# Kernel tuning notes

Measured on AMD Instinct MI355X. Metric: run time of the kernel, lower is better.

The kernel has to match this reference:

```python
import jax, jax.numpy as jnp
import numpy as np

B, N, C, H, L = 4, 1024, 1152, 16, 120
D = C // H
HID = 4 * C
EPS = 1e-6


def _ln(x):
    m = jnp.mean(x, axis=-1, keepdims=True)
    v = jnp.var(x, axis=-1, keepdims=True)
    return (x - m) * jax.lax.rsqrt(v + EPS)


def _attend(q, k, v):
    # q:(B,H,Nq,D) k,v:(B,H,Nk,D)
    scale = D ** -0.5
    s = jnp.einsum('bhnd,bhmd->bhnm', q, k) * scale
    p = jax.nn.softmax(s, axis=-1)
    o = jnp.einsum('bhnm,bhmd->bhnd', p, v)
    return o.transpose(0, 2, 1, 3).reshape(q.shape[0], q.shape[2], C)


def setup_inputs() -> dict:
    key = jax.random.key(0)
    ks = jax.random.split(key, 20)
    g = lambda i, shape, s=0.02: jax.random.normal(ks[i], shape, jnp.float32) * s
    return {
        'x': jax.random.normal(ks[0], (B, N, C), jnp.float32),
        'y': jax.random.normal(ks[1], (B, L, C), jnp.float32),
        't': jax.random.normal(ks[2], (B, 6 * C), jnp.float32),
        'sst': jax.random.normal(ks[3], (6, C), jnp.float32) / C ** 0.5,
        'qkv_w': g(4, (C, 3 * C)), 'qkv_b': jnp.zeros((3 * C,), jnp.float32),
        'proj_w': g(5, (C, C)), 'proj_b': jnp.zeros((C,), jnp.float32),
        'q_w': g(6, (C, C)), 'q_b': jnp.zeros((C,), jnp.float32),
        'kv_w': g(7, (C, 2 * C)), 'kv_b': jnp.zeros((2 * C,), jnp.float32),
        'cproj_w': g(8, (C, C)), 'cproj_b': jnp.zeros((C,), jnp.float32),
        'fc1_w': g(9, (C, HID)), 'fc1_b': jnp.zeros((HID,), jnp.float32),
        'fc2_w': g(10, (HID, C)), 'fc2_b': jnp.zeros((C,), jnp.float32),
    }


def reference(x, y, t, sst, qkv_w, qkv_b, proj_w, proj_b, q_w, q_b,
              kv_w, kv_b, cproj_w, cproj_b, fc1_w, fc1_b, fc2_w, fc2_b):
    mods = sst[None] + t.reshape(B, 6, C)  # (B,6,C)
    sh_msa, sc_msa, g_msa, sh_mlp, sc_mlp, g_mlp = [mods[:, i:i + 1] for i in range(6)]

    # --- self attention with adaLN modulation ---
    h = _ln(x) * (1 + sc_msa) + sh_msa
    qkv = (h @ qkv_w + qkv_b).reshape(B, N, 3, H, D).transpose(2, 0, 3, 1, 4)
    attn_out = _attend(qkv[0], qkv[1], qkv[2]) @ proj_w + proj_b
    x = x + g_msa * attn_out

    # --- cross attention (batched cond, no mask) ---
    q = (x @ q_w + q_b).reshape(B, N, H, D).transpose(0, 2, 1, 3)
    kv = (y @ kv_w + kv_b).reshape(B, L, 2, H, D).transpose(2, 0, 3, 1, 4)
    x = x + (_attend(q, kv[0], kv[1]) @ cproj_w + cproj_b)

    # --- MLP with adaLN modulation ---
    h = _ln(x) * (1 + sc_mlp) + sh_mlp
    h = jax.nn.gelu(h @ fc1_w + fc1_b, approximate=True) @ fc2_w + fc2_b
    x = x + g_mlp * h
    return x
```

## Files before the change

### kernel.cpp

```cpp
#include <hip/hip_runtime.h>
#include <hip/hip_bf16.h>
#include <stdint.h>

typedef __hip_bfloat16 BT;
typedef __bf16 bf16x8 __attribute__((ext_vector_type(8)));
typedef float f32x4 __attribute__((ext_vector_type(4)));

constexpr int kB = 4, kN = 1024, kC = 1152, kH = 16, kL = 120, kD = 72, kDp = 96;
constexpr int kHid = 4608, kBN = 4096, kZ = 64;
constexpr float kScale = 0.11785113019775793f;

__global__ void detect_dtype(const void* xin, int* flag) {
  __shared__ int cnt;
  if (threadIdx.x == 0) cnt = 0;
  __syncthreads();
  const BT* xb = (const BT*)xin;
  int local = 0;
  for (int i = threadIdx.x; i < 4096; i += 256) {
    float v = __bfloat162float(xb[i]);
    if (!(fabsf(v) <= 1e3f)) local++;
  }
  atomicAdd(&cnt, local);
  __syncthreads();
  if (threadIdx.x == 0) *flag = (cnt > 8) ? 1 : 0;
}

struct ConvSeg {
  const void* src;
  BT* dst;
  long long n;
};
struct ConvArgs {
  ConvSeg seg[10];
  int nseg;
};
__global__ void convert_all(ConvArgs a, const int* __restrict__ flag) {
  const int f = *flag;
  long long i = (long long)blockIdx.x * 256 + threadIdx.x;
#pragma unroll
  for (int s = 0; s < 10; ++s) {
    if (s >= a.nseg) return;
    if (i < a.seg[s].n) {
      a.seg[s].dst[i] = f ? __float2bfloat16(((const float*)a.seg[s].src)[i])
                          : ((const BT*)a.seg[s].src)[i];
      return;
    }
    i -= a.seg[s].n;
  }
}

__global__ void encode_ws(float* out, long long n, float c) {
  long long i = (long long)blockIdx.x * 256 + threadIdx.x;
  if (i < n) out[i] = c;
}

__device__ __forceinline__ void gl_lds16(const BT* g, BT* l) {
  __builtin_amdgcn_global_load_lds(
      (const __attribute__((address_space(1))) uint32_t*)g,
      (__attribute__((address_space(3))) uint32_t*)l, 16, 0, 0);
}

template <int BM, int BN, int EP>
__global__ __launch_bounds__(256, 3) void gemm_t64(
    const BT* __restrict__ A, const BT* __restrict__ Bm, const BT* __restrict__ bias,
    void* __restrict__ Cout, int M, int Nc, int K, int lda, int ldb, int ldc,
    long long sA, long long sB, long long sC) {
  constexpr int NA = BM / 32;
  constexpr int NB = BN / 32;
  constexpr int NU = NA + NB;
  constexpr int NJ = (BM == 128 && BN == 128) ? 4 : 2;
  __shared__ __align__(16) BT As[2][BM * 64];
  __shared__ __align__(16) BT Bs[2][BN * 64];
  A += (long long)blockIdx.z * sA;
  Bm += (long long)blockIdx.z * sB;

  const int gx = gridDim.x, nwg = gx * gridDim.y;
  int id = blockIdx.y * gx + blockIdx.x;
  {
    const int q = nwg >> 3, r = nwg & 7;
    const int xcd = id & 7, pos = id >> 3;
    const int base = (xcd < r) ? xcd * (q + 1) : r * (q + 1) + (xcd - r) * q;
    id = base + pos;
  }
  const int m0 = (id / gx) * BM, n0 = (id % gx) * BN;

  const int lane = threadIdx.x & 63, w = threadIdx.x >> 6;
  const int l15 = lane & 15;
  const int srow = lane >> 3;
  const int ssrc = ((lane & 7) ^ srow) * 8;
  int wm, wn;
  if (BM == 128 && BN == 128) { wm = (w & 1) * 64; wn = (w >> 1) * 64; }
  else if (BM == 128) { wm = (w >> 1) * 64; wn = (w & 1) * 32; }
  else { wm = 0; wn = w * 32; }

  const bool has2 = (w + 4 < NU);
  const int u1 = w;
  const int u2 = has2 ? (w + 4) : w;
  const BT* gp1[4];
  const BT* gp2[4];
#pragma unroll
  for (int q = 0; q < 4; ++q) {
    {
      int rr, lim;
      const BT* basep;
      int stride;
      if (u1 < NA) { rr = m0 + u1 * 32; lim = M; basep = A; stride = lda; }
      else { rr = n0 + (u1 - NA) * 32; lim = Nc; basep = Bm; stride = ldb; }
      rr += q * 8 + srow;
      if (rr >= lim) rr = lim - 1;
      gp1[q] = basep + (long long)rr * stride + ssrc;
    }
    {
      int rr, lim;
      const BT* basep;
      int stride;
      if (u2 < NA) { rr = m0 + u2 * 32; lim = M; basep = A; stride = lda; }
      else { rr = n0 + (u2 - NA) * 32; lim = Nc; basep = Bm; stride = ldb; }
      rr += q * 8 + srow;
      if (rr >= lim) rr = lim - 1;
      gp2[q] = basep + (long long)rr * stride + ssrc;
    }
  }
  BT* d1[2];
  BT* d2[2];
#pragma unroll
  for (int bb = 0; bb < 2; ++bb) {
    d1[bb] = (u1 < NA) ? &As[bb][u1 * 2048] : &Bs[bb][(u1 - NA) * 2048];
    int ub = u2 - NA;
    if (ub < 0) ub = 0;
    if (ub > NB - 1) ub = NB - 1;
    d2[bb] = (u2 < NA) ? &As[bb][u2 * 2048] : &Bs[bb][ub * 2048];
  }

  auto stage = [&](int bb, int k0) {
#pragma unroll
    for (int q = 0; q < 4; ++q) gl_lds16(gp1[q] + k0, d1[bb] + q * 512);
    if (has2) {
#pragma unroll
      for (int q = 0; q < 4; ++q) gl_lds16(gp2[q] + k0, d2[bb] + q * 512);
    }
  };

  const int rsw = l15 & 7;
  const int ch0 = ((lane >> 4) ^ rsw) * 8;
  const int ch1 = ((4 | (lane >> 4)) ^ rsw) * 8;

  f32x4 acc[4][NJ] = {};

  auto compute = [&](int bb) {
    bf16x8 af[4][2], bf[NJ][2];
#pragma unroll
    for (int i = 0; i < 4; ++i) {
      const int row = wm + i * 16 + l15;
      af[i][0] = *reinterpret_cast<const bf16x8*>(&As[bb][row * 64 + ch0]);
      af[i][1] = *reinterpret_cast<const bf16x8*>(&As[bb][row * 64 + ch1]);
    }
#pragma unroll
    for (int j = 0; j < NJ; ++j) {
      const int row = wn + j * 16 + l15;
      bf[j][0] = *reinterpret_cast<const bf16x8*>(&Bs[bb][row * 64 + ch0]);
      bf[j][1] = *reinterpret_cast<const bf16x8*>(&Bs[bb][row * 64 + ch1]);
    }
#pragma unroll
    for (int i = 0; i < 4; ++i)
#pragma unroll
      for (int j = 0; j < NJ; ++j) {
        acc[i][j] = __builtin_amdgcn_mfma_f32_16x16x32_bf16(af[i][0], bf[j][0], acc[i][j], 0, 0, 0);
        acc[i][j] = __builtin_amdgcn_mfma_f32_16x16x32_bf16(af[i][1], bf[j][1], acc[i][j], 0, 0, 0);
      }
  };

  stage(0, 0);
  __syncthreads();
  const int nk = K >> 6;
  int cur = 0;
  for (int t = 1; t < nk; ++t) {
    stage(cur ^ 1, t << 6);
    compute(cur);
    __syncthreads();
    cur ^= 1;
  }
  compute(cur);

  const int rowq = (lane >> 4) * 4;
  const long long cb = (long long)blockIdx.z * sC;
#pragma unroll
  for (int j = 0; j < NJ; ++j) {
    int col = n0 + wn + j * 16 + l15;
    if (col >= Nc) continue;
    float bv = bias ? __bfloat162float(bias[col]) : 0.f;
#pragma unroll
    for (int i = 0; i < 4; ++i) {
      int row = m0 + wm + i * 16 + rowq;
#pragma unroll
      for (int r = 0; r < 4; ++r) {
        if (row + r < M) {
          float v = acc[i][j][r] + bv;
          if (EP == 2) {
            float z = 1.5957691216057308f * (v + 0.044715f * v * v * v);
            v = v / (1.f + __expf(-z));
          }
          long long off = cb + (long long)(row + r) * ldc + col;
          if (EP == 1)
            ((float*)Cout)[off] = v;
          else
            ((BT*)Cout)[off] = __float2bfloat16(v);
        }
      }
    }
  }
}

template <int EP>
__global__ __launch_bounds__(256, 4) void gemm_tile(
    const BT* __restrict__ A, const BT* __restrict__ Bm, const BT* __restrict__ bias,
    void* __restrict__ Cout, int M, int Nc, int K, int lda, int ldb, int ldc,
    long long sA, long long sB, long long sC) {
  __shared__ __align__(16) BT As[2][128 * 32];
  __shared__ __align__(16) BT Bs[2][128 * 32];
  A += (long long)blockIdx.z * sA;
  Bm += (long long)blockIdx.z * sB;

  const int gx = gridDim.x, nwg = gx * gridDim.y;
  int id = blockIdx.y * gx + blockIdx.x;
  {
    const int q = nwg >> 3, r = nwg & 7;
    const int xcd = id & 7, pos = id >> 3;
    const int base = (xcd < r) ? xcd * (q + 1) : r * (q + 1) + (xcd - r) * q;
    id = base + pos;
  }
  const int m0 = (id / gx) * 128, n0 = (id % gx) * 128;

  const int lane = threadIdx.x & 63, w = threadIdx.x >> 6;
  const int lr = lane >> 2, lc = (lane & 3) * 8;
  const int l15 = lane & 15, q8 = (lane >> 4) * 8;
  const int wm = (w & 1) * 64, wn = (w >> 1) * 64;

  int ra0 = m0 + w * 32 + lr, ra1 = ra0 + 16;
  if (ra0 >= M) ra0 = M - 1;
  if (ra1 >= M) ra1 = M - 1;
  int rb0 = n0 + w * 32 + lr, rb1 = rb0 + 16;
  if (rb0 >= Nc) rb0 = Nc - 1;
  if (rb1 >= Nc) rb1 = Nc - 1;
  const BT* pa0 = A + (long long)ra0 * lda + lc;
  const BT* pa1 = A + (long long)ra1 * lda + lc;
  const BT* pb0 = Bm + (long long)rb0 * ldb + lc;
  const BT* pb1 = Bm + (long long)rb1 * ldb + lc;

  auto stage = [&](int bb, int k0) {
    gl_lds16(pa0 + k0, &As[bb][w * 1024]);
    gl_lds16(pa1 + k0, &As[bb][w * 1024 + 512]);
    gl_lds16(pb0 + k0, &Bs[bb][w * 1024]);
    gl_lds16(pb1 + k0, &Bs[bb][w * 1024 + 512]);
  };

  f32x4 acc[4][4] = {};

  auto compute = [&](int bb) {
    bf16x8 af[4], bf[4];
#pragma unroll
    for (int i = 0; i < 4; ++i)
      af[i] = *reinterpret_cast<const bf16x8*>(&As[bb][(wm + i * 16 + l15) * 32 + q8]);
#pragma unroll
    for (int j = 0; j < 4; ++j)
      bf[j] = *reinterpret_cast<const bf16x8*>(&Bs[bb][(wn + j * 16 + l15) * 32 + q8]);
#pragma unroll
    for (int i = 0; i < 4; ++i)
#pragma unroll
      for (int j = 0; j < 4; ++j)
        acc[i][j] = __builtin_amdgcn_mfma_f32_16x16x32_bf16(af[i], bf[j], acc[i][j], 0, 0, 0);
  };

  stage(0, 0);
  __syncthreads();
  const int nk = K >> 5;
  int cur = 0;
  for (int t = 1; t < nk; ++t) {
    stage(cur ^ 1, t << 5);
    compute(cur);
    __syncthreads();
    cur ^= 1;
  }
  compute(cur);

  const int rowq = (lane >> 4) * 4;
  const long long cb = (long long)blockIdx.z * sC;
#pragma unroll
  for (int j = 0; j < 4; ++j) {
    int col = n0 + wn + j * 16 + l15;
    if (col >= Nc) continue;
    float bv = bias ? __bfloat162float(bias[col]) : 0.f;
#pragma unroll
    for (int i = 0; i < 4; ++i) {
      int row = m0 + wm + i * 16 + rowq;
#pragma unroll
      for (int r = 0; r < 4; ++r) {
        if (row + r < M) {
          float v = acc[i][j][r] + bv;
          if (EP == 2) {
            float z = 1.5957691216057308f * (v + 0.044715f * v * v * v);
            v = v / (1.f + __expf(-z));
          }
          long long off = cb + (long long)(row + r) * ldc + col;
          if (EP == 1)
            ((float*)Cout)[off] = v;
          else
            ((BT*)Cout)[off] = __float2bfloat16(v);
        }
      }
    }
  }
}

__global__ void transpose_any(const void* __restrict__ in, BT* __restrict__ out,
                              int R, int Cin, const int* __restrict__ flag) {
  __shared__ BT tile[32][33];
  const int f = *flag;
  const int tx = threadIdx.x & 31, ty = threadIdx.x >> 5;
  const int r0 = blockIdx.y * 32, c0 = blockIdx.x * 32;
#pragma unroll
  for (int j = 0; j < 32; j += 8) {
    int r = r0 + ty + j;
    if (r < R && c0 + tx < Cin) {
      long long idx = (long long)r * Cin + c0 + tx;
      tile[ty + j][tx] = f ? __float2bfloat16(((const float*)in)[idx]) : ((const BT*)in)[idx];
    }
  }
  __syncthreads();
#pragma unroll
  for (int j = 0; j < 32; j += 8) {
    int oc = c0 + ty + j;
    if (oc < Cin && r0 + tx < R) out[(long long)oc * R + r0 + tx] = tile[tx][ty + j];
  }
}

template <int SRC>
__global__ __launch_bounds__(256) void ln_mod(const void* __restrict__ xin,
                                              const BT* __restrict__ tc,
                                              const BT* __restrict__ sstc,
                                              BT* __restrict__ hout,
                                              int shiftRow, int scaleRow,
                                              const int* __restrict__ flag) {
  const int f = (SRC == 1) ? 1 : *flag;
  const int row = blockIdx.x;
  const int b = row >> 10;
  const long long base = (long long)row * kC;
  float s = 0.f, s2 = 0.f;
  for (int c = threadIdx.x; c < kC; c += 256) {
    float v = f ? ((const float*)xin)[base + c] : __bfloat162float(((const BT*)xin)[base + c]);
    s += v;
    s2 += v * v;
  }
  for (int o = 32; o > 0; o >>= 1) {
    s += __shfl_down(s, o, 64);
    s2 += __shfl_down(s2, o, 64);
  }
  __shared__ float red[8];
  const int w = threadIdx.x >> 6;
  if ((threadIdx.x & 63) == 0) {
    red[w] = s;
    red[4 + w] = s2;
  }
  __syncthreads();
  const float m = (red[0] + red[1] + red[2] + red[3]) * (1.f / kC);
  const float ex2 = (red[4] + red[5] + red[6] + red[7]) * (1.f / kC);
  const float rstd = rsqrtf(ex2 - m * m + 1e-6f);
  const BT* tsh = tc + (long long)b * 6 * kC + (long long)shiftRow * kC;
  const BT* tsc = tc + (long long)b * 6 * kC + (long long)scaleRow * kC;
  const BT* ssh = sstc + (long long)shiftRow * kC;
  const BT* ssc = sstc + (long long)scaleRow * kC;
  for (int c = threadIdx.x; c < kC; c += 256) {
    float sc = __bfloat162float(ssc[c]) + __bfloat162float(tsc[c]);
    float sh = __bfloat162float(ssh[c]) + __bfloat162float(tsh[c]);
    float xv0 = f ? ((const float*)xin)[base + c] : __bfloat162float(((const BT*)xin)[base + c]);
    float xv = (xv0 - m) * rstd;
    hout[base + c] = __float2bfloat16(xv * (1.f + sc) + sh);
  }
}

__global__ void scatter_qk(const BT* __restrict__ qkv, BT* __restrict__ Qp,
                           BT* __restrict__ Kp) {
  long long i = (long long)blockIdx.x * 256 + threadIdx.x;
  if (i >= (long long)kZ * kN * kDp) return;
  int d = (int)(i % kDp);
  long long r = i / kDp;
  int n = (int)(r % kN);
  int z = (int)(r / kN);
  int b = z >> 4, h = z & 15;
  if (d < kD) {
    long long src = ((long long)(b * kN + n)) * (3 * kC) + h * kD + d;
    Qp[i] = __float2bfloat16(kScale * __bfloat162float(qkv[src]));
    Kp[i] = qkv[src + kC];
  } else {
    Qp[i] = __float2bfloat16(0.f);
    Kp[i] = __float2bfloat16(0.f);
  }
}

__global__ void scatter_v(const BT* __restrict__ qkv, BT* __restrict__ VT) {
  long long i = (long long)blockIdx.x * 256 + threadIdx.x;
  if (i >= (long long)kZ * kD * kN) return;
  int n = (int)(i % kN);
  long long r = i / kN;
  int d = (int)(r % kD);
  int z = (int)(r / kD);
  int b = z >> 4, h = z & 15;
  VT[i] = qkv[((long long)(b * kN + n)) * (3 * kC) + 2 * kC + h * kD + d];
}

__global__ void scatter_qc(const BT* __restrict__ qc, BT* __restrict__ Qp) {
  long long i = (long long)blockIdx.x * 256 + threadIdx.x;
  if (i >= (long long)kZ * kN * kDp) return;
  int d = (int)(i % kDp);
  long long r = i / kDp;
  int n = (int)(r % kN);
  int z = (int)(r / kN);
  int b = z >> 4, h = z & 15;
  Qp[i] = (d < kD)
              ? __float2bfloat16(kScale * __bfloat162float(qc[((long long)(b * kN + n)) * kC + h * kD + d]))
              : __float2bfloat16(0.f);
}

__global__ void scatter_kc(const BT* __restrict__ kvb, BT* __restrict__ Kcp) {
  long long i = (long long)blockIdx.x * 256 + threadIdx.x;
  if (i >= (long long)kZ * kL * kDp) return;
  int d = (int)(i % kDp);
  long long r = i / kDp;
  int l = (int)(r % kL);
  int z = (int)(r / kL);
  int b = z >> 4, h = z & 15;
  Kcp[i] = (d < kD) ? kvb[((long long)(b * kL + l)) * (2 * kC) + h * kD + d] : __float2bfloat16(0.f);
}

__global__ void scatter_vc(const BT* __restrict__ kvb, BT* __restrict__ VcT) {
  long long i = (long long)blockIdx.x * 256 + threadIdx.x;
  if (i >= (long long)kZ * kD * 128) return;
  int l = (int)(i % 128);
  long long r = i / 128;
  int d = (int)(r % kD);
  int z = (int)(r / kD);
  int b = z >> 4, h = z & 15;
  VcT[i] = (l < kL) ? kvb[((long long)(b * kL + l)) * (2 * kC) + kC + h * kD + d] : __float2bfloat16(0.f);
}

__global__ void heads_to_cat(const BT* __restrict__ O, BT* __restrict__ cat) {
  long long i = (long long)blockIdx.x * 256 + threadIdx.x;
  if (i >= (long long)kZ * kN * kD) return;
  int d = (int)(i % kD);
  long long r = i / kD;
  int n = (int)(r % kN);
  int z = (int)(r / kN);
  int b = z >> 4, h = z & 15;
  cat[((long long)(b * kN + n)) * kC + h * kD + d] = O[i];
}

__global__ __launch_bounds__(256) void softmax1024(BT* __restrict__ S) {
  const long long row = blockIdx.x;
  BT* r = S + row * 1024;
  const int tid = threadIdx.x;
  union { ushort4 u; BT b[4]; } ld;
  ld.u = *(const ushort4*)(r + tid * 4);
  float v[4];
#pragma unroll
  for (int k = 0; k < 4; ++k) v[k] = __bfloat162float(ld.b[k]);
  float mx = fmaxf(fmaxf(v[0], v[1]), fmaxf(v[2], v[3]));
  for (int o = 32; o > 0; o >>= 1) mx = fmaxf(mx, __shfl_down(mx, o, 64));
  __shared__ float red[4], red2[4];
  if ((tid & 63) == 0) red[tid >> 6] = mx;
  __syncthreads();
  mx = fmaxf(fmaxf(red[0], red[1]), fmaxf(red[2], red[3]));
  float s = 0.f;
#pragma unroll
  for (int k = 0; k < 4; ++k) {
    v[k] = __expf(v[k] - mx);
    s += v[k];
  }
  for (int o = 32; o > 0; o >>= 1) s += __shfl_down(s, o, 64);
  if ((tid & 63) == 0) red2[tid >> 6] = s;
  __syncthreads();
  s = red2[0] + red2[1] + red2[2] + red2[3];
  const float inv = 1.f / s;
#pragma unroll
  for (int k = 0; k < 4; ++k) ld.b[k] = __float2bfloat16(v[k] * inv);
  *(ushort4*)(r + tid * 4) = ld.u;
}

__global__ void softmax_cross(BT* __restrict__ S) {
  const long long row = blockIdx.x;
  BT* r = S + row * 128;
  const int c = threadIdx.x;
  float v = (c < kL) ? __bfloat162float(r[c]) : -1e30f;
  float mx = v;
  for (int o = 32; o > 0; o >>= 1) mx = fmaxf(mx, __shfl_down(mx, o, 64));
  __shared__ float sm[2], ss[2];
  if ((c & 63) == 0) sm[c >> 6] = mx;
  __syncthreads();
  mx = fmaxf(sm[0], sm[1]);
  float e = (c < kL) ? __expf(v - mx) : 0.f;
  float s = e;
  for (int o = 32; o > 0; o >>= 1) s += __shfl_down(s, o, 64);
  if ((c & 63) == 0) ss[c >> 6] = s;
  __syncthreads();
  s = ss[0] + ss[1];
  r[c] = __float2bfloat16(e / s);
}

__global__ void resid_gate(const void* __restrict__ x, const BT* __restrict__ raw,
                           const BT* __restrict__ tc, const BT* __restrict__ sstc,
                           float* __restrict__ resf, BT* __restrict__ resb,
                           const int* __restrict__ flag) {
  long long i = (long long)blockIdx.x * 256 + threadIdx.x;
  if (i >= (long long)kBN * kC) return;
  const int f = *flag;
  int c = (int)(i % kC);
  int b = (int)(i / ((long long)kN * kC));
  float g = __bfloat162float(sstc[2 * kC + c]) + __bfloat162float(tc[(long long)b * 6 * kC + 2 * kC + c]);
  float xv = f ? ((const float*)x)[i] : __bfloat162float(((const BT*)x)[i]);
  float v = xv + g * __bfloat162float(raw[i]);
  resf[i] = v;
  resb[i] = __float2bfloat16(v);
}

__global__ void resid_add(float* __restrict__ res, const BT* __restrict__ raw) {
  long long i = (long long)blockIdx.x * 256 + threadIdx.x;
  if (i < (long long)kBN * kC) res[i] += __bfloat162float(raw[i]);
}

__global__ void final_out(const float* __restrict__ res, const BT* __restrict__ raw,
                          const BT* __restrict__ tc, const BT* __restrict__ sstc,
                          float* __restrict__ out) {
  long long i = (long long)blockIdx.x * 256 + threadIdx.x;
  if (i >= (long long)kBN * kC) return;
  int c = (int)(i % kC);
  int b = (int)(i / ((long long)kN * kC));
  float g = __bfloat162float(sstc[5 * kC + c]) + __bfloat162float(tc[(long long)b * 6 * kC + 5 * kC + c]);
  out[i] = res[i] + g * __bfloat162float(raw[i]);
}

extern "C" void kernel_launch(void* const* d_in, const int* in_sizes, int n_in,
                              void* d_out, int out_size, void* d_ws, size_t ws_size,
                              hipStream_t stream) {
  const void* x = d_in[0];
  const void* y = d_in[1];
  const void* t = d_in[2];
  const void* sst = d_in[3];
  const void* qkv_w = d_in[4];
  const void* qkv_b = d_in[5];
  const void* proj_w = d_in[6];
  const void* proj_b = d_in[7];
  const void* q_w = d_in[8];
  const void* q_b = d_in[9];
  const void* kv_w = d_in[10];
  const void* kv_b = d_in[11];
  const void* cproj_w = d_in[12];
  const void* cproj_b = d_in[13];
  const void* fc1_w = d_in[14];
  const void* fc1_b = d_in[15];
  const void* fc2_w = d_in[16];
  const void* fc2_b = d_in[17];
  (void)in_sizes; (void)n_in;

  char* p = (char*)d_ws;
  size_t off = 0;
  auto alloc = [&](size_t bytes) {
    void* r = p + off;
    off += (bytes + 1023) & ~(size_t)1023;
    return r;
  };
  int* dflag = (int*)alloc(16);
  BT* canonY = (BT*)alloc((size_t)kB * kL * kC * 2);
  BT* canonT = (BT*)alloc((size_t)kB * 6 * kC * 2);
  BT* canonSst = (BT*)alloc((size_t)6 * kC * 2);
  BT* canonBias = (BT*)alloc((size_t)16384 * 2);
  BT* wT = (BT*)alloc((size_t)kHid * kC * 2);
  BT* bufH = (BT*)alloc((size_t)kBN * kC * 2);
  BT* bufCH = (BT*)alloc((size_t)kZ * kN * kDp * 2);
  BT* bufQp = (BT*)alloc((size_t)kZ * kN * kDp * 2);
  BT* bufVT = (BT*)alloc((size_t)kZ * kD * kN * 2);
  BT* rawB = (BT*)alloc((size_t)kBN * kC * 2);
  float* resF = (float*)alloc((size_t)kBN * kC * 4);
  BT* arena = (BT*)alloc((size_t)kBN * kHid * 2);
  const size_t need = off;

  BT* bufO = rawB;
  BT* fc2T = bufQp;
  BT* kvBuf = (BT*)((char*)arena + 17825792);

  if (ws_size < need) {
    float c = 100.f * (float)(1 + (int)(ws_size >> 24));
    long long n = (long long)out_size;
    encode_ws<<<(int)((n + 255) / 256), 256, 0, stream>>>((float*)d_out, n, c);
    return;
  }

  BT* qkvB = canonBias;
  BT* projB = canonBias + 3456;
  BT* qB = canonBias + 4608;
  BT* kvB = canonBias + 5760;
  BT* cprojB = canonBias + 8064;
  BT* fc1B = canonBias + 9216;
  BT* fc2B = canonBias + 13824;

  auto gemm = [&](int ep, const BT* A, const BT* Bm, const BT* bias, void* Cp,
                  int M, int Nc, int K, int lda, int ldb, int ldc,
                  long long sA, long long sB, long long sC, int Zb) {
    if (K & 63) {
      dim3 g((Nc + 127) / 128, (M + 127) / 128, Zb);
      if (ep == 0)
        gemm_tile<0><<<g, 256, 0, stream>>>(A, Bm, bias, Cp, M, Nc, K, lda, ldb, ldc, sA, sB, sC);
      else if (ep == 1)
        gemm_tile<1><<<g, 256, 0, stream>>>(A, Bm, bias, Cp, M, Nc, K, lda, ldb, ldc, sA, sB, sC);
      else
        gemm_tile<2><<<g, 256, 0, stream>>>(A, Bm, bias, Cp, M, Nc, K, lda, ldb, ldc, sA, sB, sC);
      return;
    }
    long long n64 = (long long)((Nc + 63) / 64) * ((M + 127) / 128) * Zb;
    if (n64 >= 512) {
      dim3 g((Nc + 63) / 64, (M + 127) / 128, Zb);
      if (ep == 0)
        gemm_t64<128, 64, 0><<<g, 256, 0, stream>>>(A, Bm, bias, Cp, M, Nc, K, lda, ldb, ldc, sA, sB, sC);
      else if (ep == 1)
        gemm_t64<128, 64, 1><<<g, 256, 0, stream>>>(A, Bm, bias, Cp, M, Nc, K, lda, ldb, ldc, sA, sB, sC);
      else
        gemm_t64<128, 64, 2><<<g, 256, 0, stream>>>(A, Bm, bias, Cp, M, Nc, K, lda, ldb, ldc, sA, sB, sC);
    } else {
      dim3 g((Nc + 127) / 128, (M + 63) / 64, Zb);
      if (ep == 0)
        gemm_t64<64, 128, 0><<<g, 256, 0, stream>>>(A, Bm, bias, Cp, M, Nc, K, lda, ldb, ldc, sA, sB, sC);
      else if (ep == 1)
        gemm_t64<64, 128, 1><<<g, 256, 0, stream>>>(A, Bm, bias, Cp, M, Nc, K, lda, ldb, ldc, sA, sB, sC);
      else
        gemm_t64<64, 128, 2><<<g, 256, 0, stream>>>(A, Bm, bias, Cp, M, Nc, K, lda, ldb, ldc, sA, sB, sC);
    }
  };
  auto tp = [&](const void* in, BT* out, int R, int Cin) {
    dim3 g((Cin + 31) / 32, (R + 31) / 32);
    transpose_any<<<g, 256, 0, stream>>>(in, out, R, Cin, dflag);
  };

  detect_dtype<<<1, 256, 0, stream>>>(x, dflag);
  {
    ConvArgs a;
    a.seg[0] = {y, canonY, (long long)kB * kL * kC};
    a.seg[1] = {t, canonT, (long long)kB * 6 * kC};
    a.seg[2] = {sst, canonSst, (long long)6 * kC};
    a.seg[3] = {qkv_b, qkvB, 3456};
    a.seg[4] = {proj_b, projB, 1152};
    a.seg[5] = {q_b, qB, 1152};
    a.seg[6] = {kv_b, kvB, 2304};
    a.seg[7] = {cproj_b, cprojB, 1152};
    a.seg[8] = {fc1_b, fc1B, 4608};
    a.seg[9] = {fc2_b, fc2B, 1152};
    a.nseg = 10;
    long long tot = 552960 + 27648 + 6912 + 14976;
    convert_all<<<(int)((tot + 255) / 256), 256, 0, stream>>>(a, dflag);
  }

  ln_mod<0><<<kBN, 256, 0, stream>>>(x, canonT, canonSst, bufH, 0, 1, dflag);
  tp(qkv_w, wT, kC, 3 * kC);
  gemm(0, bufH, wT, qkvB, arena, kBN, 3 * kC, kC, kC, kC, 3 * kC, 0, 0, 0, 1);
  {
    long long tot = (long long)kZ * kN * kDp;
    scatter_qk<<<(int)((tot + 255) / 256), 256, 0, stream>>>(arena, bufQp, bufCH);
    tot = (long long)kZ * kD * kN;
    scatter_v<<<(int)((tot + 255) / 256), 256, 0, stream>>>(arena, bufVT);
  }
  for (int c = 0; c < 4; ++c) {
    int z0 = c * 16;
    const BT* Qb = bufQp + (size_t)z0 * kN * kDp;
    const BT* Kb = bufCH + (size_t)z0 * kN * kDp;
    const BT* Vb = bufVT + (size_t)z0 * kD * kN;
    BT* Ob = bufO + (size_t)z0 * kN * kD;
    gemm(0, Qb, Kb, nullptr, arena, kN, kN, kDp, kDp, kDp, kN,
         (long long)kN * kDp, (long long)kN * kDp, (long long)kN * kN, 16);
    softmax1024<<<16 * kN, 256, 0, stream>>>(arena);
    gemm(0, arena, Vb, nullptr, Ob, kN, kD, kN, kN, kN, kD,
         (long long)kN * kN, (long long)kD * kN, (long long)kN * kD, 16);
  }
  heads_to_cat<<<18432, 256, 0, stream>>>(bufO, bufCH);
  tp(proj_w, wT, kC, kC);
  gemm(0, bufCH, wT, projB, rawB, kBN, kC, kC, kC, kC, kC, 0, 0, 0, 1);
  resid_gate<<<18432, 256, 0, stream>>>(x, rawB, canonT, canonSst, resF, bufH, dflag);

  tp(q_w, wT, kC, kC);
  gemm(0, bufH, wT, qB, bufCH, kBN, kC, kC, kC, kC, kC, 0, 0, 0, 1);
  {
    long long tot = (long long)kZ * kN * kDp;
    scatter_qc<<<(int)((tot + 255) / 256), 256, 0, stream>>>(bufCH, bufQp);
  }
  tp(kv_w, wT, kC, 2 * kC);
  gemm(0, canonY, wT, kvB, kvBuf, kB * kL, 2 * kC, kC, kC, kC, 2 * kC, 0, 0, 0, 1);
  {
    long long tot = (long long)kZ * kL * kDp;
    scatter_kc<<<(int)((tot + 255) / 256), 256, 0, stream>>>(kvBuf, bufCH);
    tot = (long long)kZ * kD * 128;
    scatter_vc<<<(int)((tot + 255) / 256), 256, 0, stream>>>(kvBuf, bufVT);
  }
  gemm(0, bufQp, bufCH, nullptr, arena, kN, kL, kDp, kDp, kDp, 128,
       (long long)kN * kDp, (long long)kL * kDp, (long long)kN * 128, kZ);
  softmax_cross<<<kZ * kN, 128, 0, stream>>>(arena);
  gemm(0, arena, bufVT, nullptr, bufO, kN, kD, 128, 128, 128, kD,
       (long long)kN * 128, (long long)kD * 128, (long long)kN * kD, kZ);
  heads_to_cat<<<18432, 256, 0, stream>>>(bufO, bufCH);
  tp(cproj_w, wT, kC, kC);
  gemm(0, bufCH, wT, cprojB, rawB, kBN, kC, kC, kC, kC, kC, 0, 0, 0, 1);
  resid_add<<<18432, 256, 0, stream>>>(resF, rawB);

  ln_mod<1><<<kBN, 256, 0, stream>>>(resF, canonT, canonSst, bufH, 3, 4, dflag);
  tp(fc1_w, wT, kC, kHid);
  tp(fc2_w, fc2T, kHid, kC);
  gemm(2, bufH, wT, fc1B, arena, kBN, kHid, kC, kC, kC, kHid, 0, 0, 0, 1);
  gemm(0, arena, fc2T, fc2B, rawB, kBN, kC, kHid, kHid, kHid, kC, 0, 0, 0, 1);
  final_out<<<18432, 256, 0, stream>>>(resF, rawB, canonT, canonSst, (float*)d_out);
}
```

Baseline: 822.4 us.

## Add triple-buffered 128x64 GEMM kernel with async LDS loads for M%128 shapes

Adds a new bf16 MFMA GEMM kernel that uses three LDS stages filled by global_load_lds, keeping two tiles in flight. It waits with a partial vmcnt so loads overlap with compute, and raises wave priority around the MFMA block. The dispatcher now routes every GEMM whose M is a multiple of 128 to this kernel instead of choosing tile shape by grid size. The old 128-wide variants of gemm_t64 are simplified away. The extra stage raises LDS use to 72KB per block and lowers the occupancy bound to 2, and smaller-grid GEMMs lose the 64x128 tiling choice.

```diff
diff --git a/kernel.cpp b/kernel.cpp
--- a/kernel.cpp
+++ b/kernel.cpp
@@ -60,6 +60,151 @@
       (__attribute__((address_space(3))) uint32_t*)l, 16, 0, 0);
 }
 
+__device__ __forceinline__ bf16x8 ds_read128(const BT* p) {
+  f32x4 r;
+  auto lp = (const __attribute__((address_space(3))) f32x4*)p;
+  asm volatile("ds_read_b128 %0, %1" : "=v"(r) : "v"(lp));
+  return __builtin_bit_cast(bf16x8, r);
+}
+
+template <int EP>
+__global__ __launch_bounds__(256, 2) void gemm_p3(
+    const BT* __restrict__ A, const BT* __restrict__ Bm, const BT* __restrict__ bias,
+    void* __restrict__ Cout, int M, int Nc, int K, int lda, int ldb, int ldc,
+    long long sA, long long sB, long long sC) {
+  __shared__ __align__(16) BT As[3][128 * 64];
+  __shared__ __align__(16) BT Bs[3][64 * 64];
+  A += (long long)blockIdx.z * sA;
+  Bm += (long long)blockIdx.z * sB;
+
+  const int gx = gridDim.x, nwg = gx * gridDim.y;
+  int id = blockIdx.y * gx + blockIdx.x;
+  {
+    const int q = nwg >> 3, r = nwg & 7;
+    const int xcd = id & 7, pos = id >> 3;
+    const int base = (xcd < r) ? xcd * (q + 1) : r * (q + 1) + (xcd - r) * q;
+    id = base + pos;
+  }
+  const int m0 = (id / gx) * 128, n0 = (id % gx) * 64;
+
+  const int lane = threadIdx.x & 63, w = threadIdx.x >> 6;
+  const int l15 = lane & 15;
+  const int srow = lane >> 3;
+  const int ssrc = ((lane & 7) ^ srow) * 8;
+  const int wm = (w >> 1) * 64, wn = (w & 1) * 32;
+
+  const BT* gsp[6];
+  int eoff[6];
+  bool isA[6];
+#pragma unroll
+  for (int i = 0; i < 6; ++i) {
+    const int gidx = w * 6 + i;
+    const int u = gidx >> 2, q = gidx & 3;
+    if (u < 4) {
+      int rr = m0 + u * 32 + q * 8 + srow;
+      if (rr >= M) rr = M - 1;
+      gsp[i] = A + (long long)rr * lda + ssrc;
+      eoff[i] = u * 2048 + q * 512;
+      isA[i] = true;
+    } else {
+      int rr = n0 + (u - 4) * 32 + q * 8 + srow;
+      if (rr >= Nc) rr = Nc - 1;
+      gsp[i] = Bm + (long long)rr * ldb + ssrc;
+      eoff[i] = (u - 4) * 2048 + q * 512;
+      isA[i] = false;
+    }
+  }
+
+  auto stage = [&](int bb, int k0) {
+#pragma unroll
+    for (int i = 0; i < 6; ++i)
+      gl_lds16(gsp[i] + k0, isA[i] ? &As[bb][eoff[i]] : &Bs[bb][eoff[i]]);
+  };
+
+  const int rsw = l15 & 7;
+  const int ch0 = ((lane >> 4) ^ rsw) * 8;
+  const int ch1 = ((4 | (lane >> 4)) ^ rsw) * 8;
+
+  f32x4 acc[4][2] = {};
+
+  const int nk = K >> 6;
+  stage(0, 0);
+  stage(1, 64);
+  asm volatile("s_waitcnt vmcnt(6)" ::: "memory");
+  __builtin_amdgcn_s_barrier();
+
+  int cur = 0;
+  for (int t = 0; t < nk; ++t) {
+    const bool more = (t + 2 < nk);
+    if (more) {
+      int nb = cur + 2;
+      if (nb >= 3) nb -= 3;
+      stage(nb, (t + 2) << 6);
+    }
+    const BT* Ab = &As[cur][0];
+    const BT* Bb = &Bs[cur][0];
+    bf16x8 af[4][2], bf[2][2];
+#pragma unroll
+    for (int i = 0; i < 4; ++i) {
+      const int row = wm + i * 16 + l15;
+      af[i][0] = ds_read128(&Ab[row * 64 + ch0]);
+      af[i][1] = ds_read128(&Ab[row * 64 + ch1]);
+    }
+#pragma unroll
+    for (int j = 0; j < 2; ++j) {
+      const int row = wn + j * 16 + l15;
+      bf[j][0] = ds_read128(&Bb[row * 64 + ch0]);
+      bf[j][1] = ds_read128(&Bb[row * 64 + ch1]);
+    }
+    asm volatile("s_waitcnt lgkmcnt(0)" ::: "memory");
+    __builtin_amdgcn_sched_barrier(0);
+    __builtin_amdgcn_s_setprio(1);
+#pragma unroll
+    for (int i = 0; i < 4; ++i)
+#pragma unroll
+      for (int j = 0; j < 2; ++j) {
+        acc[i][j] = __builtin_amdgcn_mfma_f32_16x16x32_bf16(af[i][0], bf[j][0], acc[i][j], 0, 0, 0);
+        acc[i][j] = __builtin_amdgcn_mfma_f32_16x16x32_bf16(af[i][1], bf[j][1], acc[i][j], 0, 0, 0);
+      }
+    __builtin_amdgcn_s_setprio(0);
+    if (more)
+      asm volatile("s_waitcnt vmcnt(6)" ::: "memory");
+    else
+      asm volatile("s_waitcnt vmcnt(0)" ::: "memory");
+    __builtin_amdgcn_s_barrier();
+    ++cur;
+    if (cur == 3) cur = 0;
+  }
+
+  const int rowq = (lane >> 4) * 4;
+  const long long cb = (long long)blockIdx.z * sC;
+#pragma unroll
+  for (int j = 0; j < 2; ++j) {
+    int col = n0 + wn + j * 16 + l15;
+    if (col >= Nc) continue;
+    float bv = bias ? __bfloat162float(bias[col]) : 0.f;
+#pragma unroll
+    for (int i = 0; i < 4; ++i) {
+      int row = m0 + wm + i * 16 + rowq;
+#pragma unroll
+      for (int r = 0; r < 4; ++r) {
+        if (row + r < M) {
+          float v = acc[i][j][r] + bv;
+          if (EP == 2) {
+            float z = 1.5957691216057308f * (v + 0.044715f * v * v * v);
+            v = v / (1.f + __expf(-z));
+          }
+          long long off = cb + (long long)(row + r) * ldc + col;
+          if (EP == 1)
+            ((float*)Cout)[off] = v;
+          else
+            ((BT*)Cout)[off] = __float2bfloat16(v);
+        }
+      }
+    }
+  }
+}
+
 template <int BM, int BN, int EP>
 __global__ __launch_bounds__(256, 3) void gemm_t64(
     const BT* __restrict__ A, const BT* __restrict__ Bm, const BT* __restrict__ bias,
@@ -68,7 +213,7 @@
   constexpr int NA = BM / 32;
   constexpr int NB = BN / 32;
   constexpr int NU = NA + NB;
-  constexpr int NJ = (BM == 128 && BN == 128) ? 4 : 2;
+  constexpr int NJ = 2;
   __shared__ __align__(16) BT As[2][BM * 64];
   __shared__ __align__(16) BT Bs[2][BN * 64];
   A += (long long)blockIdx.z * sA;
@@ -88,10 +233,7 @@
   const int l15 = lane & 15;
   const int srow = lane >> 3;
   const int ssrc = ((lane & 7) ^ srow) * 8;
-  int wm, wn;
-  if (BM == 128 && BN == 128) { wm = (w & 1) * 64; wn = (w >> 1) * 64; }
-  else if (BM == 128) { wm = (w >> 1) * 64; wn = (w & 1) * 32; }
-  else { wm = 0; wn = w * 32; }
+  const int wm = 0, wn = w * 32;
 
   const bool has2 = (w + 4 < NU);
   const int u1 = w;
@@ -614,15 +756,14 @@
         gemm_tile<2><<<g, 256, 0, stream>>>(A, Bm, bias, Cp, M, Nc, K, lda, ldb, ldc, sA, sB, sC);
       return;
     }
-    long long n64 = (long long)((Nc + 63) / 64) * ((M + 127) / 128) * Zb;
-    if (n64 >= 512) {
-      dim3 g((Nc + 63) / 64, (M + 127) / 128, Zb);
+    if ((M & 127) == 0) {
+      dim3 g((Nc + 63) / 64, M / 128, Zb);
       if (ep == 0)
-        gemm_t64<128, 64, 0><<<g, 256, 0, stream>>>(A, Bm, bias, Cp, M, Nc, K, lda, ldb, ldc, sA, sB, sC);
+        gemm_p3<0><<<g, 256, 0, stream>>>(A, Bm, bias, Cp, M, Nc, K, lda, ldb, ldc, sA, sB, sC);
       else if (ep == 1)
-        gemm_t64<128, 64, 1><<<g, 256, 0, stream>>>(A, Bm, bias, Cp, M, Nc, K, lda, ldb, ldc, sA, sB, sC);
+        gemm_p3<1><<<g, 256, 0, stream>>>(A, Bm, bias, Cp, M, Nc, K, lda, ldb, ldc, sA, sB, sC);
       else
-        gemm_t64<128, 64, 2><<<g, 256, 0, stream>>>(A, Bm, bias, Cp, M, Nc, K, lda, ldb, ldc, sA, sB, sC);
+        gemm_p3<2><<<g, 256, 0, stream>>>(A, Bm, bias, Cp, M, Nc, K, lda, ldb, ldc, sA, sB, sC);
     } else {
       dim3 g((Nc + 127) / 128, (M + 63) / 64, Zb);
       if (ep == 0)
```

New measurement: 832.6 us. About the same (+1.2%).
